# Kernel tuning notes

Hardware: AMD Instinct MI355X
Metric: run time of the kernel (lower is better)

## Reference

```python
import jax, jax.numpy as jnp
import numpy as np

N = 100000   # num nodes
E = 1000000  # num edges
IN, H, OUT = 128, 64, 64
THR = 0.1      # lcs_threshold
LN_EPS = 1e-5


def setup_inputs() -> dict:
    key = jax.random.key(0)
    ks = jax.random.split(key, 8)
    x = jax.random.normal(ks[0], (N, IN), dtype=jnp.float32)
    edge_index = jax.random.randint(ks[1], (2, E), 0, N, dtype=jnp.int32)
    W1 = jax.random.normal(ks[2], (IN, H), dtype=jnp.float32) / np.float32(np.sqrt(IN))
    b1 = jnp.zeros((H,), jnp.float32)
    W2 = jax.random.normal(ks[3], (H, OUT), dtype=jnp.float32) / np.float32(np.sqrt(H))
    b2 = jnp.zeros((OUT,), jnp.float32)
    ln_gamma = jnp.ones((H,), jnp.float32)
    ln_beta = jnp.zeros((H,), jnp.float32)
    return {"x": x, "W1": W1, "b1": b1, "W2": W2, "b2": b2,
            "ln_gamma": ln_gamma, "ln_beta": ln_beta, "edge_index": edge_index}


def _gcn_conv(h_in, W, b, src, dst, ew, n):
    """PyG GCNConv: D^-1/2 (A+I) D^-1/2 (h_in @ W) + b, with edge weights ew.
    Masked edges (ew=0) contribute neither messages nor degree -> equivalent to
    filtering them out."""
    h = h_in @ W                                   # [n, d_out]
    deg = jax.ops.segment_sum(ew, dst, num_segments=n) + 1.0  # +1 self-loop
    dis = jax.lax.rsqrt(deg)                       # deg >= 1, finite
    norm = dis[src] * dis[dst] * ew                # [E]
    agg = jax.ops.segment_sum(h[src] * norm[:, None], dst, num_segments=n)
    agg = agg + h * (dis * dis)[:, None]           # self-loop term
    return agg + b


def _layer_norm(h, gamma, beta):
    mu = jnp.mean(h, axis=-1, keepdims=True)
    var = jnp.mean(jnp.square(h - mu), axis=-1, keepdims=True)
    return (h - mu) * jax.lax.rsqrt(var + LN_EPS) * gamma + beta


def reference(x, W1, b1, W2, b2, ln_gamma, ln_beta, edge_index):
    src, dst = edge_index[0], edge_index[1]
    n = x.shape[0]
    ones_e = jnp.ones((src.shape[0],), x.dtype)

    # layer 0: no LCS filtering (i == 0)
    h = _gcn_conv(x, W1, b1, src, dst, ones_e, n)
    h = _layer_norm(h, ln_gamma, ln_beta)
    h = jax.nn.relu(h)  # dropout: inference mode (identity)

    # layer 1: LCS filtering via node scores = min-max normalized L2 norm
    s = jnp.linalg.norm(h, axis=1)
    s = (s - s.min()) / (s.max() - s.min() + 1e-8)
    mask = (s[dst] > THR).astype(x.dtype)

    out = _gcn_conv(h, W2, b2, src, dst, mask, n)
    return jax.nn.log_softmax(out, axis=1)
```

## Files before the change

### kernel.cpp

```cpp
#include <hip/hip_runtime.h>
#include <math.h>

#define N_NODES 100000
#define N_EDGES 1000000
#define IN_F 128
#define H_F 64
#define THRV 0.1f
#define LN_EPS 1e-5f
#define GRID_AGG 2048

#define BSHIFT 9
#define NB 196
#define BCAP 6144
#define EPB 2048
#define NPB ((N_EDGES + EPB - 1) / EPB)

static __device__ __forceinline__ float wave_sum(float x) {
  for (int o = 32; o > 0; o >>= 1) x += __shfl_xor(x, o, 64);
  return x;
}
static __device__ __forceinline__ float wave_max(float x) {
  for (int o = 32; o > 0; o >>= 1) x = fmaxf(x, __shfl_xor(x, o, 64));
  return x;
}
static __device__ __forceinline__ unsigned short f2bf(float f) {
  unsigned u = __float_as_uint(f);
  u = (u + 0x7FFFu + ((u >> 16) & 1u)) >> 16;
  return (unsigned short)u;
}
static __device__ __forceinline__ float bf2f(unsigned short b) {
  return __uint_as_float(((unsigned)b) << 16);
}


__global__ __launch_bounds__(256) void k_part(const int* __restrict__ src,
                                              const int* __restrict__ dst,
                                              int* __restrict__ bcnt,
                                              int* __restrict__ part) {
  __shared__ int h[NB];
  __shared__ int cur[NB];
  int t = threadIdx.x;
  for (int i = t; i < NB; i += 256) h[i] = 0;
  __syncthreads();
  int base = blockIdx.x * EPB;
  int d[8];
#pragma unroll
  for (int i = 0; i < 8; ++i) {
    int e = base + t + i * 256;
    d[i] = (e < N_EDGES) ? dst[e] : -1;
  }
#pragma unroll
  for (int i = 0; i < 8; ++i)
    if (d[i] >= 0) atomicAdd(&h[d[i] >> BSHIFT], 1);
  __syncthreads();
  for (int i = t; i < NB; i += 256) {
    int c = h[i];
    cur[i] = c ? atomicAdd(&bcnt[i], c) : 0;
  }
  __syncthreads();
#pragma unroll
  for (int i = 0; i < 8; ++i) {
    if (d[i] >= 0) {
      int e = base + t + i * 256;
      int b = d[i] >> BSHIFT;
      int pos = atomicAdd(&cur[b], 1);
      part[b * BCAP + pos] = src[e] | ((d[i] & 511) << 17);
    }
  }
}

__global__ __launch_bounds__(256) void k_build(
    const int* __restrict__ part, const int* __restrict__ bcnt,
    int* __restrict__ indeg, int* __restrict__ offs, float* __restrict__ dis1,
    int* __restrict__ csr_src) {
  __shared__ int cnt[512];
  __shared__ int slds[256];
  int b = blockIdx.x;
  int t = threadIdx.x;
  int beg = b * BCAP;
  int end = beg + bcnt[b];
  for (int i = t; i < 512; i += 256) cnt[i] = 0;
  __syncthreads();
  for (int i = beg + t; i < end; i += 256)
    atomicAdd(&cnt[(part[i] >> 17) & 511], 1);
  __syncthreads();
  int a0 = cnt[2 * t], a1 = cnt[2 * t + 1];
  int pairsum = a0 + a1;
  slds[t] = pairsum;
  __syncthreads();
  int val = pairsum;
  for (int o = 1; o < 256; o <<= 1) {
    int y = (t >= o) ? slds[t - o] : 0;
    __syncthreads();
    val += y;
    slds[t] = val;
    __syncthreads();
  }
  int ex = val - pairsum;
  int off0 = ex, off1 = ex + a0;
  cnt[2 * t] = off0;
  cnt[2 * t + 1] = off1;
  int node0 = (b << BSHIFT) + 2 * t;
  if (node0 < N_NODES) {
    indeg[node0] = a0;
    offs[node0] = beg + off0;
    dis1[node0] = rsqrtf((float)a0 + 1.f);
  }
  if (node0 + 1 < N_NODES) {
    indeg[node0 + 1] = a1;
    offs[node0 + 1] = beg + off1;
    dis1[node0 + 1] = rsqrtf((float)a1 + 1.f);
  }
  __syncthreads();
  for (int i = beg + t; i < end; i += 256) {
    int p = part[i];
    int loc = (p >> 17) & 511;
    int pos = atomicAdd(&cnt[loc], 1);
    csr_src[beg + pos] = p & 131071;
  }
}

template <int K, bool BF16OUT>
__global__ __launch_bounds__(256) void k_gemm(const float* __restrict__ X,
                                              const float* __restrict__ W,
                                              const float* __restrict__ scale,
                                              void* __restrict__ Yv, int nrows) {
  __shared__ __align__(16) float Ws[K][64];
  int t = threadIdx.x;
  for (int idx = t; idx < K * 16; idx += 256)
    ((float4*)&Ws[0][0])[idx] = ((const float4*)W)[idx];
  __syncthreads();

  int lane = t & 63;
  int wid = t >> 6;
  int tx = lane & 15, ty = lane >> 4;
  int rbase = blockIdx.x * 64 + wid * 16 + ty * 4;
  int r[4];
#pragma unroll
  for (int i = 0; i < 4; ++i) {
    int g = rbase + i;
    r[i] = (g < nrows) ? g : (nrows - 1);
  }
  int c0 = tx * 4;
  float acc[4][4] = {};

#pragma unroll 2
  for (int k = 0; k < K; k += 4) {
    float xv[4][4], wv[4][4];
#pragma unroll
    for (int i = 0; i < 4; ++i)
      *(float4*)xv[i] = *(const float4*)(X + (size_t)r[i] * K + k);
#pragma unroll
    for (int j = 0; j < 4; ++j)
      *(float4*)wv[j] = *(const float4*)&Ws[k + j][c0];
#pragma unroll
    for (int i = 0; i < 4; ++i)
#pragma unroll
      for (int kk = 0; kk < 4; ++kk)
#pragma unroll
        for (int j = 0; j < 4; ++j)
          acc[i][j] = fmaf(xv[i][kk], wv[kk][j], acc[i][j]);
  }

#pragma unroll
  for (int i = 0; i < 4; ++i) {
    int gr = rbase + i;
    if (gr < nrows) {
      float sc = scale[gr];
      if constexpr (BF16OUT) {
        ushort4 o;
        o.x = f2bf(acc[i][0] * sc);
        o.y = f2bf(acc[i][1] * sc);
        o.z = f2bf(acc[i][2] * sc);
        o.w = f2bf(acc[i][3] * sc);
        *(ushort4*)((unsigned short*)Yv + (size_t)gr * 64 + c0) = o;
      } else {
        float4 o;
        o.x = acc[i][0] * sc;
        o.y = acc[i][1] * sc;
        o.z = acc[i][2] * sc;
        o.w = acc[i][3] * sc;
        *(float4*)((float*)Yv + (size_t)gr * 64 + c0) = o;
      }
    }
  }
}

__global__ __launch_bounds__(256) void k_agg1(
    const float* __restrict__ h1p, const int* __restrict__ offs,
    const int* __restrict__ indeg, const int* __restrict__ csr_src,
    const float* __restrict__ dis1, const float* __restrict__ b1,
    const float* __restrict__ gamma, const float* __restrict__ beta,
    float* __restrict__ h, float* __restrict__ s, int* __restrict__ smm_i) {
  int lane = threadIdx.x & 63;
  int wid = blockIdx.x * 4 + (threadIdx.x >> 6);
  int nw = gridDim.x * 4;
  float bmin = __builtin_inff(), bmax = -__builtin_inff();
  float b1l = b1[lane], gl = gamma[lane], bl = beta[lane];

  int v = wid;
  int beg = 0, deg = 0;
  float disv = 0.f, self = 0.f;
  if (v < N_NODES) {
    beg = offs[v];
    deg = indeg[v];
    disv = dis1[v];
    self = h1p[v * 64 + lane];
  }
  while (v < N_NODES) {
    int vn = v + nw;
    int begN = 0, degN = 0;
    float disN = 0.f, selfN = 0.f;
    if (vn < N_NODES) {
      begN = offs[vn];
      degN = indeg[vn];
      disN = dis1[vn];
      selfN = h1p[vn * 64 + lane];
    }
    float acc = self;
    for (int c = 0; c < deg; c += 64) {
      int m = deg - c;
      if (m > 64) m = 64;
      int ul = (lane < m) ? csr_src[beg + c + lane] : 0;
      int j = 0;
      for (; j + 8 <= m; j += 8) {
        int u0 = __shfl(ul, j + 0), u1 = __shfl(ul, j + 1);
        int u2 = __shfl(ul, j + 2), u3 = __shfl(ul, j + 3);
        int u4 = __shfl(ul, j + 4), u5 = __shfl(ul, j + 5);
        int u6 = __shfl(ul, j + 6), u7 = __shfl(ul, j + 7);
        float a0 = h1p[u0 * 64 + lane], a1 = h1p[u1 * 64 + lane];
        float a2 = h1p[u2 * 64 + lane], a3 = h1p[u3 * 64 + lane];
        float a4 = h1p[u4 * 64 + lane], a5 = h1p[u5 * 64 + lane];
        float a6 = h1p[u6 * 64 + lane], a7 = h1p[u7 * 64 + lane];
        acc += ((a0 + a1) + (a2 + a3)) + ((a4 + a5) + (a6 + a7));
      }
      for (; j < m; ++j) {
        int u = __shfl(ul, j);
        acc += h1p[u * 64 + lane];
      }
    }
    acc = disv * acc + b1l;
    float mu = wave_sum(acc) * (1.f / 64.f);
    float d = acc - mu;
    float var = wave_sum(d * d) * (1.f / 64.f);
    float hn = d * rsqrtf(var + LN_EPS) * gl + bl;
    hn = fmaxf(hn, 0.f);
    h[v * 64 + lane] = hn;
    float sv = sqrtf(wave_sum(hn * hn));
    if (lane == 0) s[v] = sv;
    bmin = fminf(bmin, sv);
    bmax = fmaxf(bmax, sv);
    v = vn;
    beg = begN;
    deg = degN;
    disv = disN;
    self = selfN;
  }
  __shared__ float lmin[4], lmax[4];
  if ((threadIdx.x & 63) == 0) {
    lmin[threadIdx.x >> 6] = bmin;
    lmax[threadIdx.x >> 6] = bmax;
  }
  __syncthreads();
  if (threadIdx.x == 0) {
    float mn = fminf(fminf(lmin[0], lmin[1]), fminf(lmin[2], lmin[3]));
    float mx = fmaxf(fmaxf(lmax[0], lmax[1]), fmaxf(lmax[2], lmax[3]));
    atomicMin(&smm_i[0], __float_as_int(mn));
    atomicMax(&smm_i[1], __float_as_int(mx));
  }
}

__global__ void k_dis2(const float* __restrict__ s, const int* __restrict__ smm_i,
                       const int* __restrict__ indeg, float* __restrict__ dis2) {
  int v = blockIdx.x * blockDim.x + threadIdx.x;
  if (v < N_NODES) {
    float smin = __int_as_float(smm_i[0]);
    float smax = __int_as_float(smm_i[1]);
    float inv = 1.f / (smax - smin + 1e-8f);
    float sn = (s[v] - smin) * inv;
    float d = (sn > THRV) ? (float)indeg[v] : 0.f;
    dis2[v] = rsqrtf(d + 1.f);
  }
}

__global__ __launch_bounds__(256) void k_agg2(
    const unsigned short* __restrict__ h2b, const int* __restrict__ offs,
    const int* __restrict__ indeg, const int* __restrict__ csr_src,
    const float* __restrict__ s, const int* __restrict__ smm_i,
    const float* __restrict__ dis2, const float* __restrict__ b2,
    float* __restrict__ out) {
  int lane = threadIdx.x & 63;
  int wid = blockIdx.x * 4 + (threadIdx.x >> 6);
  int nw = gridDim.x * 4;
  float smin = __int_as_float(smm_i[0]);
  float smax = __int_as_float(smm_i[1]);
  float inv = 1.f / (smax - smin + 1e-8f);
  float b2l = b2[lane];

  int v = wid;
  int beg = 0, deg = 0;
  float disv = 0.f, self = 0.f, sn = 0.f;
  if (v < N_NODES) {
    beg = offs[v];
    deg = indeg[v];
    disv = dis2[v];
    self = bf2f(h2b[v * 64 + lane]);
    sn = (s[v] - smin) * inv;
  }
  while (v < N_NODES) {
    int vn = v + nw;
    int begN = 0, degN = 0;
    float disN = 0.f, selfN = 0.f, snN = 0.f;
    if (vn < N_NODES) {
      begN = offs[vn];
      degN = indeg[vn];
      disN = dis2[vn];
      selfN = bf2f(h2b[vn * 64 + lane]);
      snN = (s[vn] - smin) * inv;
    }
    float acc = self;
    if (sn > THRV) {
      for (int c = 0; c < deg; c += 64) {
        int m = deg - c;
        if (m > 64) m = 64;
        int ul = (lane < m) ? csr_src[beg + c + lane] : 0;
        int j = 0;
        for (; j + 8 <= m; j += 8) {
          int u0 = __shfl(ul, j + 0), u1 = __shfl(ul, j + 1);
          int u2 = __shfl(ul, j + 2), u3 = __shfl(ul, j + 3);
          int u4 = __shfl(ul, j + 4), u5 = __shfl(ul, j + 5);
          int u6 = __shfl(ul, j + 6), u7 = __shfl(ul, j + 7);
          float a0 = bf2f(h2b[u0 * 64 + lane]), a1 = bf2f(h2b[u1 * 64 + lane]);
          float a2 = bf2f(h2b[u2 * 64 + lane]), a3 = bf2f(h2b[u3 * 64 + lane]);
          float a4 = bf2f(h2b[u4 * 64 + lane]), a5 = bf2f(h2b[u5 * 64 + lane]);
          float a6 = bf2f(h2b[u6 * 64 + lane]), a7 = bf2f(h2b[u7 * 64 + lane]);
          acc += ((a0 + a1) + (a2 + a3)) + ((a4 + a5) + (a6 + a7));
        }
        for (; j < m; ++j) {
          int u = __shfl(ul, j);
          acc += bf2f(h2b[u * 64 + lane]);
        }
      }
    }
    acc = disv * acc + b2l;
    float m = wave_max(acc);
    float p = expf(acc - m);
    float sum = wave_sum(p);
    out[v * 64 + lane] = acc - m - logf(sum);
    v = vn;
    beg = begN;
    deg = degN;
    disv = disN;
    self = selfN;
    sn = snN;
  }
}

extern "C" void kernel_launch(void* const* d_in, const int* in_sizes, int n_in,
                              void* d_out, int out_size, void* d_ws, size_t ws_size,
                              hipStream_t stream) {
  const float* x = (const float*)d_in[0];
  const float* W1 = (const float*)d_in[1];
  const float* b1 = (const float*)d_in[2];
  const float* W2 = (const float*)d_in[3];
  const float* b2 = (const float*)d_in[4];
  const float* gamma = (const float*)d_in[5];
  const float* beta = (const float*)d_in[6];
  const int* ei = (const int*)d_in[7];
  const int* src = ei;
  const int* dst = ei + N_EDGES;
  float* out = (float*)d_out;

  char* ws = (char*)d_ws;
  size_t off = 0;
  auto alloc = [&](size_t bytes) {
    void* p = ws + off;
    off += (bytes + 255) & ~(size_t)255;
    return p;
  };
  int* indeg = (int*)alloc(N_NODES * 4);
  int* offs = (int*)alloc(N_NODES * 4);
  int* bcnt = (int*)alloc(NB * 4);
  int* smm_i = (int*)alloc(256);
  int* csr_src = (int*)alloc((size_t)NB * BCAP * 4);
  float* s = (float*)alloc(N_NODES * 4);
  float* dis1 = (float*)alloc(N_NODES * 4);
  float* dis2 = (float*)alloc(N_NODES * 4);
  float* h1 = (float*)alloc((size_t)N_NODES * 64 * 4);
  float* h = (float*)alloc((size_t)N_NODES * 64 * 4);
  int* part = (int*)h1;
  unsigned short* h2b = (unsigned short*)h1;
  (void)ws_size;
  (void)n_in;
  (void)in_sizes;
  (void)out_size;

  hipMemsetAsync(bcnt, 0, NB * 4, stream);
  hipMemsetAsync(&smm_i[0], 0x7F, 4, stream);
  hipMemsetAsync(&smm_i[1], 0x00, 4, stream);
  k_part<<<NPB, 256, 0, stream>>>(src, dst, bcnt, part);
  k_build<<<NB, 256, 0, stream>>>(part, bcnt, indeg, offs, dis1, csr_src);
  int gemm_grid = (N_NODES + 63) / 64;
  k_gemm<IN_F, false><<<gemm_grid, 256, 0, stream>>>(x, W1, dis1, h1, N_NODES);
  k_agg1<<<GRID_AGG, 256, 0, stream>>>(h1, offs, indeg, csr_src, dis1, b1, gamma,
                                       beta, h, s, smm_i);
  k_dis2<<<(N_NODES + 255) / 256, 256, 0, stream>>>(s, smm_i, indeg, dis2);
  k_gemm<H_F, true><<<gemm_grid, 256, 0, stream>>>(h, W2, dis2, h2b, N_NODES);
  k_agg2<<<GRID_AGG, 256, 0, stream>>>(h2b, offs, indeg, csr_src, s, smm_i, dis2,
                                       b2, out);
}
```

Before: 237.0 us.

## Fuse dis2 computation into GEMM and agg2, drop software prefetch in aggregations

Removes the separate k_dis2 kernel: the second GEMM now computes the masked degree normalization inline from s, the min/max pair and indeg, and k_agg2 recomputes its own rsqrt instead of loading dis2. Both aggregation kernels also drop the manual next-node prefetch and switch to a simple grid-stride loop. This saves one kernel launch and a 400KB write and read, but gives up the explicit load overlap the prefetch provided, which could hurt latency hiding in the gather loops.

```diff
diff --git a/kernel.cpp b/kernel.cpp
--- a/kernel.cpp
+++ b/kernel.cpp
@@ -120,10 +120,12 @@
   }
 }
 
-template <int K, bool BF16OUT>
+template <int K, int SCALEMODE>
 __global__ __launch_bounds__(256) void k_gemm(const float* __restrict__ X,
                                               const float* __restrict__ W,
                                               const float* __restrict__ scale,
+                                              const int* __restrict__ smm_i,
+                                              const int* __restrict__ indeg,
                                               void* __restrict__ Yv, int nrows) {
   __shared__ __align__(16) float Ws[K][64];
   int t = threadIdx.x;
@@ -162,12 +164,25 @@
           acc[i][j] = fmaf(xv[i][kk], wv[kk][j], acc[i][j]);
   }
 
+  float smin = 0.f, inv = 0.f;
+  if constexpr (SCALEMODE == 1) {
+    smin = __int_as_float(smm_i[0]);
+    float smax = __int_as_float(smm_i[1]);
+    inv = 1.f / (smax - smin + 1e-8f);
+  }
 #pragma unroll
   for (int i = 0; i < 4; ++i) {
     int gr = rbase + i;
     if (gr < nrows) {
-      float sc = scale[gr];
-      if constexpr (BF16OUT) {
+      float sc;
+      if constexpr (SCALEMODE == 1) {
+        float sn = (scale[gr] - smin) * inv;
+        float dmask = (sn > THRV) ? (float)indeg[gr] : 0.f;
+        sc = rsqrtf(dmask + 1.f);
+      } else {
+        sc = scale[gr];
+      }
+      if constexpr (SCALEMODE == 1) {
         ushort4 o;
         o.x = f2bf(acc[i][0] * sc);
         o.y = f2bf(acc[i][1] * sc);
@@ -197,27 +212,11 @@
   int nw = gridDim.x * 4;
   float bmin = __builtin_inff(), bmax = -__builtin_inff();
   float b1l = b1[lane], gl = gamma[lane], bl = beta[lane];
-
-  int v = wid;
-  int beg = 0, deg = 0;
-  float disv = 0.f, self = 0.f;
-  if (v < N_NODES) {
-    beg = offs[v];
-    deg = indeg[v];
-    disv = dis1[v];
-    self = h1p[v * 64 + lane];
-  }
-  while (v < N_NODES) {
-    int vn = v + nw;
-    int begN = 0, degN = 0;
-    float disN = 0.f, selfN = 0.f;
-    if (vn < N_NODES) {
-      begN = offs[vn];
-      degN = indeg[vn];
-      disN = dis1[vn];
-      selfN = h1p[vn * 64 + lane];
-    }
-    float acc = self;
+  for (int v = wid; v < N_NODES; v += nw) {
+    int beg = offs[v];
+    int deg = indeg[v];
+    float disv = dis1[v];
+    float acc = h1p[v * 64 + lane];
     for (int c = 0; c < deg; c += 64) {
       int m = deg - c;
       if (m > 64) m = 64;
@@ -250,11 +249,6 @@
     if (lane == 0) s[v] = sv;
     bmin = fminf(bmin, sv);
     bmax = fmaxf(bmax, sv);
-    v = vn;
-    beg = begN;
-    deg = degN;
-    disv = disN;
-    self = selfN;
   }
   __shared__ float lmin[4], lmax[4];
   if ((threadIdx.x & 63) == 0) {
@@ -270,25 +264,11 @@
   }
 }
 
-__global__ void k_dis2(const float* __restrict__ s, const int* __restrict__ smm_i,
-                       const int* __restrict__ indeg, float* __restrict__ dis2) {
-  int v = blockIdx.x * blockDim.x + threadIdx.x;
-  if (v < N_NODES) {
-    float smin = __int_as_float(smm_i[0]);
-    float smax = __int_as_float(smm_i[1]);
-    float inv = 1.f / (smax - smin + 1e-8f);
-    float sn = (s[v] - smin) * inv;
-    float d = (sn > THRV) ? (float)indeg[v] : 0.f;
-    dis2[v] = rsqrtf(d + 1.f);
-  }
-}
-
 __global__ __launch_bounds__(256) void k_agg2(
     const unsigned short* __restrict__ h2b, const int* __restrict__ offs,
     const int* __restrict__ indeg, const int* __restrict__ csr_src,
     const float* __restrict__ s, const int* __restrict__ smm_i,
-    const float* __restrict__ dis2, const float* __restrict__ b2,
-    float* __restrict__ out) {
+    const float* __restrict__ b2, float* __restrict__ out) {
   int lane = threadIdx.x & 63;
   int wid = blockIdx.x * 4 + (threadIdx.x >> 6);
   int nw = gridDim.x * 4;
@@ -296,30 +276,13 @@
   float smax = __int_as_float(smm_i[1]);
   float inv = 1.f / (smax - smin + 1e-8f);
   float b2l = b2[lane];
-
-  int v = wid;
-  int beg = 0, deg = 0;
-  float disv = 0.f, self = 0.f, sn = 0.f;
-  if (v < N_NODES) {
-    beg = offs[v];
-    deg = indeg[v];
-    disv = dis2[v];
-    self = bf2f(h2b[v * 64 + lane]);
-    sn = (s[v] - smin) * inv;
-  }
-  while (v < N_NODES) {
-    int vn = v + nw;
-    int begN = 0, degN = 0;
-    float disN = 0.f, selfN = 0.f, snN = 0.f;
-    if (vn < N_NODES) {
-      begN = offs[vn];
-      degN = indeg[vn];
-      disN = dis2[vn];
-      selfN = bf2f(h2b[vn * 64 + lane]);
-      snN = (s[vn] - smin) * inv;
-    }
-    float acc = self;
-    if (sn > THRV) {
+  for (int v = wid; v < N_NODES; v += nw) {
+    int deg = indeg[v];
+    float sn = (s[v] - smin) * inv;
+    bool on = sn > THRV;
+    float acc = bf2f(h2b[v * 64 + lane]);
+    if (on) {
+      int beg = offs[v];
       for (int c = 0; c < deg; c += 64) {
         int m = deg - c;
         if (m > 64) m = 64;
@@ -342,17 +305,12 @@
         }
       }
     }
+    float disv = rsqrtf((on ? (float)deg : 0.f) + 1.f);
     acc = disv * acc + b2l;
     float m = wave_max(acc);
     float p = expf(acc - m);
     float sum = wave_sum(p);
     out[v * 64 + lane] = acc - m - logf(sum);
-    v = vn;
-    beg = begN;
-    deg = degN;
-    disv = disN;
-    self = selfN;
-    sn = snN;
   }
 }
 
@@ -385,7 +343,6 @@
   int* csr_src = (int*)alloc((size_t)NB * BCAP * 4);
   float* s = (float*)alloc(N_NODES * 4);
   float* dis1 = (float*)alloc(N_NODES * 4);
-  float* dis2 = (float*)alloc(N_NODES * 4);
   float* h1 = (float*)alloc((size_t)N_NODES * 64 * 4);
   float* h = (float*)alloc((size_t)N_NODES * 64 * 4);
   int* part = (int*)h1;
@@ -401,11 +358,12 @@
   k_part<<<NPB, 256, 0, stream>>>(src, dst, bcnt, part);
   k_build<<<NB, 256, 0, stream>>>(part, bcnt, indeg, offs, dis1, csr_src);
   int gemm_grid = (N_NODES + 63) / 64;
-  k_gemm<IN_F, false><<<gemm_grid, 256, 0, stream>>>(x, W1, dis1, h1, N_NODES);
+  k_gemm<IN_F, 0><<<gemm_grid, 256, 0, stream>>>(x, W1, dis1, nullptr, nullptr,
+                                                 h1, N_NODES);
   k_agg1<<<GRID_AGG, 256, 0, stream>>>(h1, offs, indeg, csr_src, dis1, b1, gamma,
                                        beta, h, s, smm_i);
-  k_dis2<<<(N_NODES + 255) / 256, 256, 0, stream>>>(s, smm_i, indeg, dis2);
-  k_gemm<H_F, true><<<gemm_grid, 256, 0, stream>>>(h, W2, dis2, h2b, N_NODES);
-  k_agg2<<<GRID_AGG, 256, 0, stream>>>(h2b, offs, indeg, csr_src, s, smm_i, dis2,
-                                       b2, out);
-}
+  k_gemm<H_F, 1><<<gemm_grid, 256, 0, stream>>>(h, W2, s, smm_i, indeg, h2b,
+                                                N_NODES);
+  k_agg2<<<GRID_AGG, 256, 0, stream>>>(h2b, offs, indeg, csr_src, s, smm_i, b2,
+                                       out);
+}
```

Result: slower. 242.1 us (+2.2%).
